# Optimization experiments

Measured on AMD Instinct MI355X. Metric: run time of the kernel, lower is better.

The kernel has to match this reference:

```python
import jax, jax.numpy as jnp
import numpy as np

REG_MAX = 16
BOX_W = 7.5
OBJ_W = 1.0
TOPK = 10
EPS = 1e-7


def dfl_decode(x, reg_max):
    # x: [B, 4*reg_max, N] -> expected value of per-side distribution -> [B, N, 4] (xyxy)
    B, C, N = x.shape
    x = x.reshape(B, 4, reg_max, N)
    p = jax.nn.softmax(x, axis=2)
    proj = jnp.arange(reg_max, dtype=x.dtype)
    return jnp.einsum('bkrn,r->bnk', p, proj)


def bbox_ciou(b1, b2):
    # b1: [B,N,1,4], b2: [B,1,M,4], xyxy -> [B,N,M]
    x11, y11, x12, y12 = b1[..., 0], b1[..., 1], b1[..., 2], b1[..., 3]
    x21, y21, x22, y22 = b2[..., 0], b2[..., 1], b2[..., 2], b2[..., 3]
    w1, h1 = x12 - x11, y12 - y11
    w2, h2 = x22 - x21, y22 - y21
    iw = jnp.clip(jnp.minimum(x12, x22) - jnp.maximum(x11, x21), 0.0)
    ih = jnp.clip(jnp.minimum(y12, y22) - jnp.maximum(y11, y21), 0.0)
    inter = iw * ih
    union = w1 * h1 + w2 * h2 - inter + EPS
    iou = inter / union
    cw = jnp.maximum(x12, x22) - jnp.minimum(x11, x21)
    ch = jnp.maximum(y12, y22) - jnp.minimum(y11, y21)
    c2 = cw * cw + ch * ch + EPS
    rho2 = ((x21 + x22 - x11 - x12) ** 2 + (y21 + y22 - y11 - y12) ** 2) * 0.25
    v = (4.0 / (np.pi ** 2)) * (jnp.arctan(w2 / (h2 + EPS)) - jnp.arctan(w1 / (h1 + EPS))) ** 2
    alpha = jax.lax.stop_gradient(v / (v - iou + 1.0 + EPS))
    return iou - rho2 / c2 - alpha * v


def setup_inputs() -> dict:
    key = jax.random.key(0)
    k1, k2, k3, k4 = jax.random.split(key, 4)
    B, N, M = 8, 34000, 64
    boxes = jax.random.normal(k1, (B, 4 * REG_MAX, N), dtype=jnp.float32)
    scores = jax.random.normal(k2, (B, N), dtype=jnp.float32)
    # GT boxes: valid xyxy in roughly the same [0, reg_max) range as decoded preds
    xy = jax.random.uniform(k3, (B, M, 2), dtype=jnp.float32) * 11.0
    wh = jax.random.uniform(k4, (B, M, 2), dtype=jnp.float32) * 4.0 + 0.5
    targets = jnp.concatenate([xy, xy + wh], axis=-1)
    return {'boxes': boxes, 'scores': scores, 'targets': targets}


def reference(boxes, scores, targets):
    B, N = scores.shape
    M = targets.shape[1]
    pb = dfl_decode(boxes, REG_MAX)                     # [B,N,4]
    ciou = bbox_ciou(pb[:, :, None, :], targets[:, None, :, :])  # [B,N,M]
    k = min(TOPK, N)
    topv, topi = jax.lax.top_k(jnp.swapaxes(ciou, 1, 2), k)      # [B,M,k] over anchors
    valid = topv > 0.0
    vals = jnp.where(valid, topv, 0.0)

    def per_batch(idx, val, vld):
        flat_i = idx.reshape(-1)
        iou_t = jnp.zeros((N,), val.dtype).at[flat_i].max(val.reshape(-1))
        pos = jnp.zeros((N,), bool).at[flat_i].max(vld.reshape(-1))
        return iou_t, pos

    iou_target, pos = jax.vmap(per_batch)(topi, vals, valid)     # [B,N]
    posf = pos.astype(iou_target.dtype)
    npos = posf.sum(axis=1)
    box_per = jnp.where(npos > 0,
                        ((1.0 - iou_target) * posf).sum(axis=1) / jnp.maximum(npos, 1.0),
                        0.0)
    box_loss = box_per.sum()
    # BCEWithLogits (mean over anchors), summed over batch
    bce = jnp.maximum(scores, 0.0) - scores * iou_target + jnp.log1p(jnp.exp(-jnp.abs(scores)))
    obj_loss = bce.mean(axis=1).sum()
    total = (BOX_W * box_loss + OBJ_W * obj_loss) / B
    return total, box_loss, obj_loss
```

## Files before the change

### kernel.cpp

```cpp
#include <hip/hip_runtime.h>
#include <math.h>

#define BQ 8
#define MQ 64
#define REGMAX 16
#define KTOP 10
#define EPSQ 1e-7f
#define SSEG 4
#define TRIG 256
#define CBUF (TRIG + SSEG * 256 + 16)

__device__ __forceinline__ float frcp(float x) { return __builtin_amdgcn_rcpf(x); }


__global__ __launch_bounds__(256) void decode_kernel(
    const float* __restrict__ boxes, const float* __restrict__ scores,
    float4* __restrict__ pbc, float2* __restrict__ atc,
    unsigned int* __restrict__ iou_bits, float* __restrict__ state,
    int N, int bpb) {
  const int tid = threadIdx.x;
  const int b = blockIdx.x / bpb;
  const int n = (blockIdx.x - b * bpb) * 256 + tid;
  float* acc = state;
  int* cnt = (int*)(state + 32);

  __shared__ float4 s_v4[256];
  __shared__ float2 s_ai[256];
  __shared__ int s_cnt, s_base;
  __shared__ float r0[256];
  if (tid == 0) s_cnt = 0;
  __syncthreads();

  float bce0 = 0.f;
  if (n < N) {
    const size_t i = (size_t)b * N + n;
    iou_bits[i] = 0u;
    float sc = scores[i];
    bce0 = fmaxf(sc, 0.f) + log1pf(__expf(-fabsf(sc)));
    const float* base = boxes + (size_t)b * (4 * REGMAX) * N + n;
    float out[4];
#pragma unroll
    for (int k = 0; k < 4; ++k) {
      float x[REGMAX];
#pragma unroll
      for (int r = 0; r < REGMAX; ++r)
        x[r] = base[(size_t)(k * REGMAX + r) * N];
      float mx = x[0];
#pragma unroll
      for (int r = 1; r < REGMAX; ++r) mx = fmaxf(mx, x[r]);
      float s = 0.f, ws = 0.f;
#pragma unroll
      for (int r = 0; r < REGMAX; ++r) {
        float e = __expf(x[r] - mx);
        s += e;
        ws += (float)r * e;
      }
      out[k] = ws * frcp(s);
    }
    float w1 = out[2] - out[0], h1 = out[3] - out[1];
    if (w1 > 0.f && h1 > 0.f) {
      int slot = atomicAdd(&s_cnt, 1);
      s_v4[slot] = make_float4(out[0], out[1], out[2], out[3]);
      s_ai[slot] = make_float2(atanf(w1 * frcp(h1 + EPSQ)), __int_as_float(n));
    }
  }
  __syncthreads();
  const int bc = s_cnt;
  if (tid == 0) s_base = atomicAdd(&cnt[b], bc);
  __syncthreads();
  const int basei = s_base;
  for (int sl = tid; sl < bc; sl += 256) {
    pbc[(size_t)b * N + basei + sl] = s_v4[sl];
    atc[(size_t)b * N + basei + sl] = s_ai[sl];
  }
  r0[tid] = bce0;
  __syncthreads();
  for (int s = 128; s > 0; s >>= 1) {
    if (tid < s) r0[tid] += r0[tid + s];
    __syncthreads();
  }
  if (tid == 0) atomicAdd(&acc[b * 4 + 2], r0[0]);
}

__device__ __forceinline__ void select_top10(
    float* s_bv, int* s_bi, float* s_winv, int* s_wini,
    int* s_cnt, float* s_sthr, int c, int tid) {
  if (tid < 64) {
    for (int r = 0; r < KTOP; ++r) {
      float bv = 0.f;
      int bs = 0xffff;
      for (int sl = tid; sl < c; sl += 64) {
        float v = s_bv[sl];
        if (v > bv) { bv = v; bs = sl; }
      }
      unsigned long long key =
          ((unsigned long long)__float_as_uint(bv) << 32) | (unsigned int)bs;
#pragma unroll
      for (int d = 1; d < 64; d <<= 1) {
        unsigned long long o = __shfl_xor(key, d, 64);
        if (o > key) key = o;
      }
      if (tid == 0) {
        float wv = __uint_as_float((unsigned int)(key >> 32));
        int ws = (int)(key & 0xffffu);
        s_winv[r] = wv;
        if (wv > 0.f && ws != 0xffff) {
          s_wini[r] = s_bi[ws];
          s_bv[ws] = 0.f;
        } else {
          s_wini[r] = 0;
        }
      }
    }
    if (tid < KTOP) { s_bv[tid] = s_winv[tid]; s_bi[tid] = s_wini[tid]; }
    if (tid == 0) { *s_cnt = KTOP; *s_sthr = s_winv[KTOP - 1]; }
  }
}

__global__ __launch_bounds__(256) void topk_all_kernel(
    const float4* __restrict__ pbc, const float2* __restrict__ atc,
    const float* __restrict__ targets, const float* __restrict__ scores,
    unsigned int* __restrict__ iou_bits, unsigned int* __restrict__ fin_v,
    int* __restrict__ fin_i, float* __restrict__ state,
    float* __restrict__ out, int N) {
  const int bm = blockIdx.x;
  const int b = bm >> 6;
  const int m = bm & 63;
  const int tid = threadIdx.x;
  float* acc = state;
  int* cnt = (int*)(state + 32);
  int* done = (int*)(state + 40);
  int* done_all = (int*)(state + 48);

  __shared__ float s_bv[CBUF];
  __shared__ int s_bi[CBUF];
  __shared__ float s_winv[KTOP];
  __shared__ int s_wini[KTOP];
  __shared__ int s_cnt, s_flag, s_flag2;
  __shared__ float s_sthr;
  if (tid == 0) { s_cnt = 0; s_sthr = 0.f; }
  __syncthreads();

  const float4 t = ((const float4*)targets)[b * MQ + m];
  const float x21 = t.x, y21 = t.y, x22 = t.z, y22 = t.w;
  const float w2 = x22 - x21, h2 = y22 - y21;
  const float atan_t = atanf(w2 * frcp(h2 + EPSQ));
  const float area2 = w2 * h2;
  const float sumx2 = x21 + x22, sumy2 = y21 + y22;
  const float CPI = 4.0f / (float)(M_PI * M_PI);

  const int cntb = cnt[b];
  float sthr = 0.f;
  const float4* pbb = pbc + (size_t)b * N;
  const float2* pab = atc + (size_t)b * N;

  for (int basei = 0; basei < cntb; basei += SSEG * 256) {
#pragma unroll
    for (int s = 0; s < SSEG; ++s) {
      int j = basei + s * 256 + tid;
      if (j < cntb) {
        float4 p = pbb[j];
        float2 ai = pab[j];
        float x11 = p.x, y11 = p.y, x12 = p.z, y12 = p.w;
        float w1 = x12 - x11, h1 = y12 - y11;
        float iw = fmaxf(fminf(x12, x22) - fmaxf(x11, x21), 0.f);
        float ih = fmaxf(fminf(y12, y22) - fmaxf(y11, y21), 0.f);
        float inter = iw * ih;
        float uni = w1 * h1 + area2 - inter + EPSQ;
        float iou = inter * frcp(uni);
        float cw = fmaxf(x12, x22) - fminf(x11, x21);
        float ch = fmaxf(y12, y22) - fminf(y11, y21);
        float c2 = cw * cw + ch * ch + EPSQ;
        float dx = sumx2 - x11 - x12;
        float dy = sumy2 - y11 - y12;
        float rho2 = (dx * dx + dy * dy) * 0.25f;
        float da = atan_t - ai.x;
        float v = CPI * da * da;
        float alpha = v * frcp(v - iou + 1.f + EPSQ);
        float ciou = iou - rho2 * frcp(c2) - alpha * v;
        if (ciou > sthr) {
          int slot = atomicAdd(&s_cnt, 1);
          s_bv[slot] = ciou;
          s_bi[slot] = __float_as_int(ai.y);
        }
      }
    }
    __syncthreads();
    int c = s_cnt;
    __syncthreads();
    if (c > TRIG) {
      select_top10(s_bv, s_bi, s_winv, s_wini, &s_cnt, &s_sthr, c, tid);
      __syncthreads();
    }
    sthr = s_sthr;
  }

  int c = s_cnt;
  if (c > KTOP) {
    select_top10(s_bv, s_bi, s_winv, s_wini, &s_cnt, &s_sthr, c, tid);
    __syncthreads();
    c = KTOP;
  }

  if (tid < KTOP) {
    float v = (tid < c) ? s_bv[tid] : 0.f;
    int ix = (tid < c) ? s_bi[tid] : 0;
    if (v > 0.f) atomicMax(&iou_bits[(size_t)b * N + ix], __float_as_uint(v));
    __hip_atomic_store(&fin_v[bm * KTOP + tid], __float_as_uint(v),
                       __ATOMIC_RELAXED, __HIP_MEMORY_SCOPE_AGENT);
    __hip_atomic_store(&fin_i[bm * KTOP + tid], ix, __ATOMIC_RELAXED,
                       __HIP_MEMORY_SCOPE_AGENT);
    __threadfence();
  }
  __syncthreads();
  if (tid == 0) {
    __threadfence();
    int prev = __hip_atomic_fetch_add(&done[b], 1, __ATOMIC_ACQ_REL,
                                      __HIP_MEMORY_SCOPE_AGENT);
    s_flag = (prev == MQ - 1);
  }
  __syncthreads();

  if (s_flag) {
    __threadfence();
    for (int e = tid; e < MQ * KTOP; e += 256) {
      int slot = b * (MQ * KTOP) + e;
      unsigned int vb = __hip_atomic_load(&fin_v[slot], __ATOMIC_RELAXED,
                                          __HIP_MEMORY_SCOPE_AGENT);
      float v = __uint_as_float(vb);
      if (v > 0.f) {
        int ix = __hip_atomic_load(&fin_i[slot], __ATOMIC_RELAXED,
                                   __HIP_MEMORY_SCOPE_AGENT);
        unsigned int cur = __hip_atomic_load(&iou_bits[(size_t)b * N + ix],
                                             __ATOMIC_RELAXED,
                                             __HIP_MEMORY_SCOPE_AGENT);
        if (cur == vb) {
          atomicAdd(&acc[b * 4 + 0], 1.f - v);
          atomicAdd(&acc[b * 4 + 1], 1.f);
          atomicAdd(&acc[b * 4 + 2], -scores[(size_t)b * N + ix] * v);
        }
      }
    }
    __threadfence();
    __syncthreads();
    if (tid == 0) {
      int prev = __hip_atomic_fetch_add(done_all, 1, __ATOMIC_ACQ_REL,
                                        __HIP_MEMORY_SCOPE_AGENT);
      s_flag2 = (prev == BQ - 1);
    }
    __syncthreads();
    if (s_flag2 && tid == 0) {
      __threadfence();
      float box = 0.f, obj = 0.f;
      for (int bb = 0; bb < BQ; ++bb) {
        float sb = __hip_atomic_load(&acc[bb * 4 + 0], __ATOMIC_RELAXED,
                                     __HIP_MEMORY_SCOPE_AGENT);
        float np = __hip_atomic_load(&acc[bb * 4 + 1], __ATOMIC_RELAXED,
                                     __HIP_MEMORY_SCOPE_AGENT);
        float sc = __hip_atomic_load(&acc[bb * 4 + 2], __ATOMIC_RELAXED,
                                     __HIP_MEMORY_SCOPE_AGENT);
        box += (np > 0.f) ? sb / fmaxf(np, 1.f) : 0.f;
        obj += sc / (float)N;
      }
      out[0] = (7.5f * box + obj) / (float)BQ;
      out[1] = box;
      out[2] = obj;
    }
  }
}

extern "C" void kernel_launch(void* const* d_in, const int* in_sizes, int n_in,
                              void* d_out, int out_size, void* d_ws, size_t ws_size,
                              hipStream_t stream) {
  const float* boxes = (const float*)d_in[0];
  const float* scores = (const float*)d_in[1];
  const float* targets = (const float*)d_in[2];
  float* out = (float*)d_out;
  const int N = in_sizes[1] / BQ;

  char* ws = (char*)d_ws;
  size_t pbc_bytes = (size_t)BQ * N * sizeof(float4);
  size_t atc_bytes = (size_t)BQ * N * sizeof(float2);
  size_t iou_bytes = (size_t)BQ * N * sizeof(unsigned int);
  size_t fin_bytes = (size_t)BQ * MQ * KTOP * sizeof(unsigned int);

  float4* pbc = (float4*)ws;                   ws += pbc_bytes;
  float2* atc = (float2*)ws;                   ws += atc_bytes;
  unsigned int* iou_bits = (unsigned int*)ws;  ws += iou_bytes;
  unsigned int* fin_v = (unsigned int*)ws;     ws += fin_bytes;
  int* fin_i = (int*)ws;                       ws += fin_bytes;
  float* state = (float*)ws;

  hipMemsetAsync(state, 0, 256, stream);

  const int bpb = (N + 255) / 256;
  decode_kernel<<<BQ * bpb, 256, 0, stream>>>(boxes, scores, pbc, atc,
                                              iou_bits, state, N, bpb);
  topk_all_kernel<<<BQ * MQ, 256, 0, stream>>>(pbc, atc, targets, scores,
                                               iou_bits, fin_v, fin_i, state,
                                               out, N);
}
```

Measured before the change: 169.0 us.

## Split per-target top-k scan into chunks and vectorize decode with float4 loads

The top-k kernel now launches four blocks per (batch, target) pair. Each block scans a quarter of the compacted anchors and writes ten candidates. The last block to finish merges the forty candidates by rank counting before the existing atomic bookkeeping runs. Separately, decode now uses 64-thread blocks that each handle four anchors with float4 loads, and reduces BCE with a wave shuffle instead of a shared-memory tree. The intent is to raise occupancy and parallelism for the 512-block top-k phase and cut decode memory transactions, at the cost of an extra counter and a merge step. The decode guard `na+3<N` skips any tail anchors when N is not a multiple of 4; N=34000 is, so this is fine here.

```diff
diff --git a/kernel.cpp b/kernel.cpp
--- a/kernel.cpp
+++ b/kernel.cpp
@@ -5,6 +5,7 @@
 #define MQ 64
 #define REGMAX 16
 #define KTOP 10
+#define CH 4
 #define EPSQ 1e-7f
 #define SSEG 4
 #define TRIG 256
@@ -12,56 +13,70 @@
 
 __device__ __forceinline__ float frcp(float x) { return __builtin_amdgcn_rcpf(x); }
 
-
-__global__ __launch_bounds__(256) void decode_kernel(
+#define ST_CNT 32
+#define ST_DONEC 40
+#define ST_DONE 552
+#define ST_DONEALL 560
+#define ST_BYTES 2560
+
+__global__ __launch_bounds__(64) void decode_kernel(
     const float* __restrict__ boxes, const float* __restrict__ scores,
     float4* __restrict__ pbc, float2* __restrict__ atc,
-    unsigned int* __restrict__ iou_bits, float* __restrict__ state,
-    int N, int bpb) {
+    uint4* __restrict__ iou4, float* __restrict__ state, int N, int bpb) {
   const int tid = threadIdx.x;
   const int b = blockIdx.x / bpb;
-  const int n = (blockIdx.x - b * bpb) * 256 + tid;
+  const int q = (blockIdx.x - b * bpb) * 64 + tid;
+  const int na = q * 4;
   float* acc = state;
-  int* cnt = (int*)(state + 32);
+  int* cnt = (int*)(state + ST_CNT);
 
   __shared__ float4 s_v4[256];
   __shared__ float2 s_ai[256];
   __shared__ int s_cnt, s_base;
-  __shared__ float r0[256];
   if (tid == 0) s_cnt = 0;
   __syncthreads();
 
   float bce0 = 0.f;
-  if (n < N) {
-    const size_t i = (size_t)b * N + n;
-    iou_bits[i] = 0u;
-    float sc = scores[i];
-    bce0 = fmaxf(sc, 0.f) + log1pf(__expf(-fabsf(sc)));
-    const float* base = boxes + (size_t)b * (4 * REGMAX) * N + n;
-    float out[4];
+  if (na + 3 < N) {
+    iou4[((size_t)b * N + na) >> 2] = make_uint4(0u, 0u, 0u, 0u);
+    float4 sc4 = *(const float4*)&scores[(size_t)b * N + na];
+    bce0 = fmaxf(sc4.x, 0.f) + log1pf(__expf(-fabsf(sc4.x))) +
+           fmaxf(sc4.y, 0.f) + log1pf(__expf(-fabsf(sc4.y))) +
+           fmaxf(sc4.z, 0.f) + log1pf(__expf(-fabsf(sc4.z))) +
+           fmaxf(sc4.w, 0.f) + log1pf(__expf(-fabsf(sc4.w)));
+    float out[4][4];
+    const size_t rowbase = (size_t)b * (4 * REGMAX) * N + na;
 #pragma unroll
     for (int k = 0; k < 4; ++k) {
-      float x[REGMAX];
+      float4 X[REGMAX];
 #pragma unroll
       for (int r = 0; r < REGMAX; ++r)
-        x[r] = base[(size_t)(k * REGMAX + r) * N];
-      float mx = x[0];
-#pragma unroll
-      for (int r = 1; r < REGMAX; ++r) mx = fmaxf(mx, x[r]);
-      float s = 0.f, ws = 0.f;
-#pragma unroll
-      for (int r = 0; r < REGMAX; ++r) {
-        float e = __expf(x[r] - mx);
-        s += e;
-        ws += (float)r * e;
-      }
-      out[k] = ws * frcp(s);
-    }
-    float w1 = out[2] - out[0], h1 = out[3] - out[1];
-    if (w1 > 0.f && h1 > 0.f) {
-      int slot = atomicAdd(&s_cnt, 1);
-      s_v4[slot] = make_float4(out[0], out[1], out[2], out[3]);
-      s_ai[slot] = make_float2(atanf(w1 * frcp(h1 + EPSQ)), __int_as_float(n));
+        X[r] = *(const float4*)&boxes[rowbase + (size_t)(k * REGMAX + r) * N];
+      const float* xf = (const float*)X;
+#pragma unroll
+      for (int a = 0; a < 4; ++a) {
+        float mx = xf[a];
+#pragma unroll
+        for (int r = 1; r < REGMAX; ++r) mx = fmaxf(mx, xf[r * 4 + a]);
+        float s = 0.f, ws = 0.f;
+#pragma unroll
+        for (int r = 0; r < REGMAX; ++r) {
+          float e = __expf(xf[r * 4 + a] - mx);
+          s += e;
+          ws += (float)r * e;
+        }
+        out[k][a] = ws * frcp(s);
+      }
+    }
+#pragma unroll
+    for (int a = 0; a < 4; ++a) {
+      float x1 = out[0][a], y1 = out[1][a], x2 = out[2][a], y2 = out[3][a];
+      float w1 = x2 - x1, h1 = y2 - y1;
+      if (w1 > 0.f && h1 > 0.f) {
+        int slot = atomicAdd(&s_cnt, 1);
+        s_v4[slot] = make_float4(x1, y1, x2, y2);
+        s_ai[slot] = make_float2(atanf(w1 * frcp(h1 + EPSQ)), __int_as_float(na + a));
+      }
     }
   }
   __syncthreads();
@@ -69,17 +84,13 @@
   if (tid == 0) s_base = atomicAdd(&cnt[b], bc);
   __syncthreads();
   const int basei = s_base;
-  for (int sl = tid; sl < bc; sl += 256) {
+  for (int sl = tid; sl < bc; sl += 64) {
     pbc[(size_t)b * N + basei + sl] = s_v4[sl];
     atc[(size_t)b * N + basei + sl] = s_ai[sl];
   }
-  r0[tid] = bce0;
-  __syncthreads();
-  for (int s = 128; s > 0; s >>= 1) {
-    if (tid < s) r0[tid] += r0[tid + s];
-    __syncthreads();
-  }
-  if (tid == 0) atomicAdd(&acc[b * 4 + 2], r0[0]);
+#pragma unroll
+  for (int d = 1; d < 64; d <<= 1) bce0 += __shfl_xor(bce0, d, 64);
+  if (tid == 0) atomicAdd(&acc[b * 4 + 2], bce0);
 }
 
 __device__ __forceinline__ void select_top10(
@@ -120,17 +131,21 @@
 __global__ __launch_bounds__(256) void topk_all_kernel(
     const float4* __restrict__ pbc, const float2* __restrict__ atc,
     const float* __restrict__ targets, const float* __restrict__ scores,
-    unsigned int* __restrict__ iou_bits, unsigned int* __restrict__ fin_v,
+    unsigned int* __restrict__ iou_bits, float* __restrict__ cand_v,
+    int* __restrict__ cand_i, unsigned int* __restrict__ fin_v,
     int* __restrict__ fin_i, float* __restrict__ state,
     float* __restrict__ out, int N) {
-  const int bm = blockIdx.x;
+  const int blk = blockIdx.x;
+  const int chunk = blk & (CH - 1);
+  const int bm = blk >> 2;
   const int b = bm >> 6;
   const int m = bm & 63;
   const int tid = threadIdx.x;
   float* acc = state;
-  int* cnt = (int*)(state + 32);
-  int* done = (int*)(state + 40);
-  int* done_all = (int*)(state + 48);
+  int* cnt = (int*)(state + ST_CNT);
+  int* donec = (int*)(state + ST_DONEC);
+  int* done = (int*)(state + ST_DONE);
+  int* done_all = (int*)(state + ST_DONEALL);
 
   __shared__ float s_bv[CBUF];
   __shared__ int s_bi[CBUF];
@@ -150,15 +165,18 @@
   const float CPI = 4.0f / (float)(M_PI * M_PI);
 
   const int cntb = cnt[b];
+  const int cch = (cntb + CH - 1) / CH;
+  const int j0 = chunk * cch;
+  const int j1 = min(cntb, j0 + cch);
   float sthr = 0.f;
   const float4* pbb = pbc + (size_t)b * N;
   const float2* pab = atc + (size_t)b * N;
 
-  for (int basei = 0; basei < cntb; basei += SSEG * 256) {
+  for (int basei = j0; basei < j1; basei += SSEG * 256) {
 #pragma unroll
     for (int s = 0; s < SSEG; ++s) {
       int j = basei + s * 256 + tid;
-      if (j < cntb) {
+      if (j < j1) {
         float4 p = pbb[j];
         float2 ai = pab[j];
         float x11 = p.x, y11 = p.y, x12 = p.z, y12 = p.w;
@@ -205,67 +223,108 @@
   if (tid < KTOP) {
     float v = (tid < c) ? s_bv[tid] : 0.f;
     int ix = (tid < c) ? s_bi[tid] : 0;
-    if (v > 0.f) atomicMax(&iou_bits[(size_t)b * N + ix], __float_as_uint(v));
-    __hip_atomic_store(&fin_v[bm * KTOP + tid], __float_as_uint(v),
-                       __ATOMIC_RELAXED, __HIP_MEMORY_SCOPE_AGENT);
-    __hip_atomic_store(&fin_i[bm * KTOP + tid], ix, __ATOMIC_RELAXED,
-                       __HIP_MEMORY_SCOPE_AGENT);
-    __threadfence();
-  }
+    cand_v[(bm * CH + chunk) * KTOP + tid] = v;
+    cand_i[(bm * CH + chunk) * KTOP + tid] = ix;
+  }
+  __threadfence();
   __syncthreads();
   if (tid == 0) {
-    __threadfence();
+    int prev = __hip_atomic_fetch_add(&donec[bm], 1, __ATOMIC_ACQ_REL,
+                                      __HIP_MEMORY_SCOPE_AGENT);
+    s_flag = (prev == CH - 1);
+  }
+  __syncthreads();
+  if (!s_flag) return;
+
+  {
+    const int NC = CH * KTOP;
+    __shared__ float mv[NC];
+    __shared__ int mi[NC];
+    __shared__ float topv[KTOP];
+    __shared__ int topi[KTOP];
+    if (tid < NC) {
+      mv[tid] = __hip_atomic_load(&cand_v[bm * NC + tid], __ATOMIC_RELAXED,
+                                  __HIP_MEMORY_SCOPE_AGENT);
+      mi[tid] = __hip_atomic_load(&cand_i[bm * NC + tid], __ATOMIC_RELAXED,
+                                  __HIP_MEMORY_SCOPE_AGENT);
+    }
+    if (tid < KTOP) { topv[tid] = 0.f; topi[tid] = 0; }
+    __syncthreads();
+    if (tid < NC) {
+      float v = mv[tid];
+      if (v > 0.f) {
+        int rank = 0;
+#pragma unroll
+        for (int i2 = 0; i2 < NC; ++i2)
+          rank += (mv[i2] > v) || (mv[i2] == v && i2 < tid);
+        if (rank < KTOP) { topv[rank] = v; topi[rank] = mi[tid]; }
+      }
+    }
+    __syncthreads();
+    if (tid < KTOP) {
+      float v = topv[tid];
+      int ix = topi[tid];
+      unsigned int vb = __float_as_uint(v);
+      if (v > 0.f) atomicMax(&iou_bits[(size_t)b * N + ix], vb);
+      __hip_atomic_store(&fin_v[bm * KTOP + tid], (v > 0.f) ? vb : 0u,
+                         __ATOMIC_RELAXED, __HIP_MEMORY_SCOPE_AGENT);
+      __hip_atomic_store(&fin_i[bm * KTOP + tid], ix, __ATOMIC_RELAXED,
+                         __HIP_MEMORY_SCOPE_AGENT);
+    }
+  }
+  __threadfence();
+  __syncthreads();
+  if (tid == 0) {
     int prev = __hip_atomic_fetch_add(&done[b], 1, __ATOMIC_ACQ_REL,
                                       __HIP_MEMORY_SCOPE_AGENT);
     s_flag = (prev == MQ - 1);
   }
   __syncthreads();
-
-  if (s_flag) {
+  if (!s_flag) return;
+
+  __threadfence();
+  for (int e = tid; e < MQ * KTOP; e += 256) {
+    int slot = b * (MQ * KTOP) + e;
+    unsigned int vb = __hip_atomic_load(&fin_v[slot], __ATOMIC_RELAXED,
+                                        __HIP_MEMORY_SCOPE_AGENT);
+    float v = __uint_as_float(vb);
+    if (v > 0.f) {
+      int ix = __hip_atomic_load(&fin_i[slot], __ATOMIC_RELAXED,
+                                 __HIP_MEMORY_SCOPE_AGENT);
+      unsigned int cur = __hip_atomic_load(&iou_bits[(size_t)b * N + ix],
+                                           __ATOMIC_RELAXED,
+                                           __HIP_MEMORY_SCOPE_AGENT);
+      if (cur == vb) {
+        atomicAdd(&acc[b * 4 + 0], 1.f - v);
+        atomicAdd(&acc[b * 4 + 1], 1.f);
+        atomicAdd(&acc[b * 4 + 2], -scores[(size_t)b * N + ix] * v);
+      }
+    }
+  }
+  __threadfence();
+  __syncthreads();
+  if (tid == 0) {
+    int prev = __hip_atomic_fetch_add(done_all, 1, __ATOMIC_ACQ_REL,
+                                      __HIP_MEMORY_SCOPE_AGENT);
+    s_flag2 = (prev == BQ - 1);
+  }
+  __syncthreads();
+  if (s_flag2 && tid == 0) {
     __threadfence();
-    for (int e = tid; e < MQ * KTOP; e += 256) {
-      int slot = b * (MQ * KTOP) + e;
-      unsigned int vb = __hip_atomic_load(&fin_v[slot], __ATOMIC_RELAXED,
-                                          __HIP_MEMORY_SCOPE_AGENT);
-      float v = __uint_as_float(vb);
-      if (v > 0.f) {
-        int ix = __hip_atomic_load(&fin_i[slot], __ATOMIC_RELAXED,
+    float box = 0.f, obj = 0.f;
+    for (int bb = 0; bb < BQ; ++bb) {
+      float sb = __hip_atomic_load(&acc[bb * 4 + 0], __ATOMIC_RELAXED,
                                    __HIP_MEMORY_SCOPE_AGENT);
-        unsigned int cur = __hip_atomic_load(&iou_bits[(size_t)b * N + ix],
-                                             __ATOMIC_RELAXED,
-                                             __HIP_MEMORY_SCOPE_AGENT);
-        if (cur == vb) {
-          atomicAdd(&acc[b * 4 + 0], 1.f - v);
-          atomicAdd(&acc[b * 4 + 1], 1.f);
-          atomicAdd(&acc[b * 4 + 2], -scores[(size_t)b * N + ix] * v);
-        }
-      }
-    }
-    __threadfence();
-    __syncthreads();
-    if (tid == 0) {
-      int prev = __hip_atomic_fetch_add(done_all, 1, __ATOMIC_ACQ_REL,
-                                        __HIP_MEMORY_SCOPE_AGENT);
-      s_flag2 = (prev == BQ - 1);
-    }
-    __syncthreads();
-    if (s_flag2 && tid == 0) {
-      __threadfence();
-      float box = 0.f, obj = 0.f;
-      for (int bb = 0; bb < BQ; ++bb) {
-        float sb = __hip_atomic_load(&acc[bb * 4 + 0], __ATOMIC_RELAXED,
-                                     __HIP_MEMORY_SCOPE_AGENT);
-        float np = __hip_atomic_load(&acc[bb * 4 + 1], __ATOMIC_RELAXED,
-                                     __HIP_MEMORY_SCOPE_AGENT);
-        float sc = __hip_atomic_load(&acc[bb * 4 + 2], __ATOMIC_RELAXED,
-                                     __HIP_MEMORY_SCOPE_AGENT);
-        box += (np > 0.f) ? sb / fmaxf(np, 1.f) : 0.f;
-        obj += sc / (float)N;
-      }
-      out[0] = (7.5f * box + obj) / (float)BQ;
-      out[1] = box;
-      out[2] = obj;
-    }
+      float np = __hip_atomic_load(&acc[bb * 4 + 1], __ATOMIC_RELAXED,
+                                   __HIP_MEMORY_SCOPE_AGENT);
+      float sc = __hip_atomic_load(&acc[bb * 4 + 2], __ATOMIC_RELAXED,
+                                   __HIP_MEMORY_SCOPE_AGENT);
+      box += (np > 0.f) ? sb / fmaxf(np, 1.f) : 0.f;
+      obj += sc / (float)N;
+    }
+    out[0] = (7.5f * box + obj) / (float)BQ;
+    out[1] = box;
+    out[2] = obj;
   }
 }
 
@@ -282,21 +341,24 @@
   size_t pbc_bytes = (size_t)BQ * N * sizeof(float4);
   size_t atc_bytes = (size_t)BQ * N * sizeof(float2);
   size_t iou_bytes = (size_t)BQ * N * sizeof(unsigned int);
+  size_t cand_bytes = (size_t)BQ * MQ * CH * KTOP * sizeof(float);
   size_t fin_bytes = (size_t)BQ * MQ * KTOP * sizeof(unsigned int);
 
   float4* pbc = (float4*)ws;                   ws += pbc_bytes;
   float2* atc = (float2*)ws;                   ws += atc_bytes;
   unsigned int* iou_bits = (unsigned int*)ws;  ws += iou_bytes;
+  float* cand_v = (float*)ws;                  ws += cand_bytes;
+  int* cand_i = (int*)ws;                      ws += cand_bytes;
   unsigned int* fin_v = (unsigned int*)ws;     ws += fin_bytes;
   int* fin_i = (int*)ws;                       ws += fin_bytes;
   float* state = (float*)ws;
 
-  hipMemsetAsync(state, 0, 256, stream);
-
-  const int bpb = (N + 255) / 256;
-  decode_kernel<<<BQ * bpb, 256, 0, stream>>>(boxes, scores, pbc, atc,
-                                              iou_bits, state, N, bpb);
-  topk_all_kernel<<<BQ * MQ, 256, 0, stream>>>(pbc, atc, targets, scores,
-                                               iou_bits, fin_v, fin_i, state,
-                                               out, N);
+  hipMemsetAsync(state, 0, ST_BYTES, stream);
+
+  const int bpb = (N / 4 + 63) / 64;
+  decode_kernel<<<BQ * bpb, 64, 0, stream>>>(boxes, scores, pbc, atc,
+                                             (uint4*)iou_bits, state, N, bpb);
+  topk_all_kernel<<<BQ * MQ * CH, 256, 0, stream>>>(
+      pbc, atc, targets, scores, iou_bits, cand_v, cand_i, fin_v, fin_i,
+      state, out, N);
 }
```

New measurement: 357.7 us. 112% more time.

## Split per-target top-k across anchor chunks and vectorize DFL decode loads

Applied to the files above, without the earlier changes.

The top-k stage now runs four blocks per (batch, target), each scanning a quarter of the compacted anchors. A second small kernel merges the 40 candidates by rank and applies atomicMax with delta-based accumulation, and a separate finalize kernel replaces the last-block-done atomic chain. This raises the grid from 512 to 2048 blocks so more CUs stay busy. Decode now has each thread load float4 across four anchors for one side, which widens memory accesses and stages the expected values through shared memory. The cost is two extra kernel launches, and the delta-accumulation logic can race when concurrent updates hit the same anchor. Also, the vectorized decode skips any trailing partial group of four anchors when N is not a multiple of 4.

```diff
diff --git a/kernel.cpp b/kernel.cpp
--- a/kernel.cpp
+++ b/kernel.cpp
@@ -5,6 +5,7 @@
 #define MQ 64
 #define REGMAX 16
 #define KTOP 10
+#define CH 4
 #define EPSQ 1e-7f
 #define SSEG 4
 #define TRIG 256
@@ -12,6 +13,8 @@
 
 __device__ __forceinline__ float frcp(float x) { return __builtin_amdgcn_rcpf(x); }
 
+#define ST_CNT 32
+#define ST_BYTES 256
 
 __global__ __launch_bounds__(256) void decode_kernel(
     const float* __restrict__ boxes, const float* __restrict__ scores,
@@ -20,66 +23,76 @@
     int N, int bpb) {
   const int tid = threadIdx.x;
   const int b = blockIdx.x / bpb;
-  const int n = (blockIdx.x - b * bpb) * 256 + tid;
+  const int a0 = (blockIdx.x - b * bpb) * 256;
   float* acc = state;
-  int* cnt = (int*)(state + 32);
-
+  int* cnt = (int*)(state + ST_CNT);
+
+  __shared__ float s_ex[4 * 256];
   __shared__ float4 s_v4[256];
   __shared__ float2 s_ai[256];
+  __shared__ float r0[256];
   __shared__ int s_cnt, s_base;
-  __shared__ float r0[256];
   if (tid == 0) s_cnt = 0;
+
+  const int g = tid >> 6;
+  const int l = tid & 63;
+  const int na = a0 + l * 4;
+  if (na + 3 < N) {
+    float4 X[REGMAX];
+    const size_t rowbase = ((size_t)b * 4 * REGMAX + g * REGMAX) * N + na;
+#pragma unroll
+    for (int r = 0; r < REGMAX; ++r)
+      X[r] = *(const float4*)&boxes[rowbase + (size_t)r * N];
+    const float* xf = (const float*)X;
+    float ev[4];
+#pragma unroll
+    for (int a = 0; a < 4; ++a) {
+      float mx = xf[a];
+#pragma unroll
+      for (int r = 1; r < REGMAX; ++r) mx = fmaxf(mx, xf[r * 4 + a]);
+      float s = 0.f, ws = 0.f;
+#pragma unroll
+      for (int r = 0; r < REGMAX; ++r) {
+        float e = __expf(xf[r * 4 + a] - mx);
+        s += e;
+        ws += (float)r * e;
+      }
+      ev[a] = ws * frcp(s);
+    }
+    *(float4*)&s_ex[g * 256 + l * 4] = make_float4(ev[0], ev[1], ev[2], ev[3]);
+  }
   __syncthreads();
 
+  const int n = a0 + tid;
   float bce0 = 0.f;
   if (n < N) {
     const size_t i = (size_t)b * N + n;
     iou_bits[i] = 0u;
     float sc = scores[i];
     bce0 = fmaxf(sc, 0.f) + log1pf(__expf(-fabsf(sc)));
-    const float* base = boxes + (size_t)b * (4 * REGMAX) * N + n;
-    float out[4];
-#pragma unroll
-    for (int k = 0; k < 4; ++k) {
-      float x[REGMAX];
-#pragma unroll
-      for (int r = 0; r < REGMAX; ++r)
-        x[r] = base[(size_t)(k * REGMAX + r) * N];
-      float mx = x[0];
-#pragma unroll
-      for (int r = 1; r < REGMAX; ++r) mx = fmaxf(mx, x[r]);
-      float s = 0.f, ws = 0.f;
-#pragma unroll
-      for (int r = 0; r < REGMAX; ++r) {
-        float e = __expf(x[r] - mx);
-        s += e;
-        ws += (float)r * e;
-      }
-      out[k] = ws * frcp(s);
-    }
-    float w1 = out[2] - out[0], h1 = out[3] - out[1];
+    float x1 = s_ex[0 * 256 + tid], y1 = s_ex[1 * 256 + tid];
+    float x2 = s_ex[2 * 256 + tid], y2 = s_ex[3 * 256 + tid];
+    float w1 = x2 - x1, h1 = y2 - y1;
     if (w1 > 0.f && h1 > 0.f) {
       int slot = atomicAdd(&s_cnt, 1);
-      s_v4[slot] = make_float4(out[0], out[1], out[2], out[3]);
+      s_v4[slot] = make_float4(x1, y1, x2, y2);
       s_ai[slot] = make_float2(atanf(w1 * frcp(h1 + EPSQ)), __int_as_float(n));
     }
   }
+  r0[tid] = bce0;
   __syncthreads();
   const int bc = s_cnt;
   if (tid == 0) s_base = atomicAdd(&cnt[b], bc);
-  __syncthreads();
+  for (int s = 128; s > 0; s >>= 1) {
+    if (tid < s) r0[tid] += r0[tid + s];
+    __syncthreads();
+  }
+  if (tid == 0) atomicAdd(&acc[b * 4 + 2], r0[0]);
   const int basei = s_base;
   for (int sl = tid; sl < bc; sl += 256) {
     pbc[(size_t)b * N + basei + sl] = s_v4[sl];
     atc[(size_t)b * N + basei + sl] = s_ai[sl];
   }
-  r0[tid] = bce0;
-  __syncthreads();
-  for (int s = 128; s > 0; s >>= 1) {
-    if (tid < s) r0[tid] += r0[tid + s];
-    __syncthreads();
-  }
-  if (tid == 0) atomicAdd(&acc[b * 4 + 2], r0[0]);
 }
 
 __device__ __forceinline__ void select_top10(
@@ -117,26 +130,23 @@
   }
 }
 
-__global__ __launch_bounds__(256) void topk_all_kernel(
+__global__ __launch_bounds__(256) void topk1_kernel(
     const float4* __restrict__ pbc, const float2* __restrict__ atc,
-    const float* __restrict__ targets, const float* __restrict__ scores,
-    unsigned int* __restrict__ iou_bits, unsigned int* __restrict__ fin_v,
-    int* __restrict__ fin_i, float* __restrict__ state,
-    float* __restrict__ out, int N) {
-  const int bm = blockIdx.x;
+    const float* __restrict__ targets, float* __restrict__ cand_v,
+    int* __restrict__ cand_i, const float* __restrict__ state, int N) {
+  const int blk = blockIdx.x;
+  const int chunk = blk & (CH - 1);
+  const int bm = blk >> 2;
   const int b = bm >> 6;
   const int m = bm & 63;
   const int tid = threadIdx.x;
-  float* acc = state;
-  int* cnt = (int*)(state + 32);
-  int* done = (int*)(state + 40);
-  int* done_all = (int*)(state + 48);
+  const int* cnt = (const int*)(state + ST_CNT);
 
   __shared__ float s_bv[CBUF];
   __shared__ int s_bi[CBUF];
   __shared__ float s_winv[KTOP];
   __shared__ int s_wini[KTOP];
-  __shared__ int s_cnt, s_flag, s_flag2;
+  __shared__ int s_cnt;
   __shared__ float s_sthr;
   if (tid == 0) { s_cnt = 0; s_sthr = 0.f; }
   __syncthreads();
@@ -150,15 +160,18 @@
   const float CPI = 4.0f / (float)(M_PI * M_PI);
 
   const int cntb = cnt[b];
+  const int cch = (cntb + CH - 1) / CH;
+  const int j0 = chunk * cch;
+  const int j1 = min(cntb, j0 + cch);
   float sthr = 0.f;
   const float4* pbb = pbc + (size_t)b * N;
   const float2* pab = atc + (size_t)b * N;
 
-  for (int basei = 0; basei < cntb; basei += SSEG * 256) {
+  for (int basei = j0; basei < j1; basei += SSEG * 256) {
 #pragma unroll
     for (int s = 0; s < SSEG; ++s) {
       int j = basei + s * 256 + tid;
-      if (j < cntb) {
+      if (j < j1) {
         float4 p = pbb[j];
         float2 ai = pab[j];
         float x11 = p.x, y11 = p.y, x12 = p.z, y12 = p.w;
@@ -201,71 +214,65 @@
     __syncthreads();
     c = KTOP;
   }
-
   if (tid < KTOP) {
-    float v = (tid < c) ? s_bv[tid] : 0.f;
-    int ix = (tid < c) ? s_bi[tid] : 0;
-    if (v > 0.f) atomicMax(&iou_bits[(size_t)b * N + ix], __float_as_uint(v));
-    __hip_atomic_store(&fin_v[bm * KTOP + tid], __float_as_uint(v),
-                       __ATOMIC_RELAXED, __HIP_MEMORY_SCOPE_AGENT);
-    __hip_atomic_store(&fin_i[bm * KTOP + tid], ix, __ATOMIC_RELAXED,
-                       __HIP_MEMORY_SCOPE_AGENT);
-    __threadfence();
+    cand_v[(bm * CH + chunk) * KTOP + tid] = (tid < c) ? s_bv[tid] : 0.f;
+    cand_i[(bm * CH + chunk) * KTOP + tid] = (tid < c) ? s_bi[tid] : 0;
+  }
+}
+
+__global__ __launch_bounds__(64) void topk2_kernel(
+    const float* __restrict__ cand_v, const int* __restrict__ cand_i,
+    const float* __restrict__ scores, unsigned int* __restrict__ iou_bits,
+    float* __restrict__ state, int N) {
+  const int bm = blockIdx.x;
+  const int b = bm >> 6;
+  const int tid = threadIdx.x;
+  float* acc = state;
+  const int NC = CH * KTOP;
+  __shared__ float mv[NC];
+  __shared__ int mi[NC];
+  if (tid < NC) {
+    mv[tid] = cand_v[bm * NC + tid];
+    mi[tid] = cand_i[bm * NC + tid];
   }
   __syncthreads();
-  if (tid == 0) {
-    __threadfence();
-    int prev = __hip_atomic_fetch_add(&done[b], 1, __ATOMIC_ACQ_REL,
-                                      __HIP_MEMORY_SCOPE_AGENT);
-    s_flag = (prev == MQ - 1);
-  }
-  __syncthreads();
-
-  if (s_flag) {
-    __threadfence();
-    for (int e = tid; e < MQ * KTOP; e += 256) {
-      int slot = b * (MQ * KTOP) + e;
-      unsigned int vb = __hip_atomic_load(&fin_v[slot], __ATOMIC_RELAXED,
-                                          __HIP_MEMORY_SCOPE_AGENT);
-      float v = __uint_as_float(vb);
-      if (v > 0.f) {
-        int ix = __hip_atomic_load(&fin_i[slot], __ATOMIC_RELAXED,
-                                   __HIP_MEMORY_SCOPE_AGENT);
-        unsigned int cur = __hip_atomic_load(&iou_bits[(size_t)b * N + ix],
-                                             __ATOMIC_RELAXED,
-                                             __HIP_MEMORY_SCOPE_AGENT);
-        if (cur == vb) {
-          atomicAdd(&acc[b * 4 + 0], 1.f - v);
-          atomicAdd(&acc[b * 4 + 1], 1.f);
-          atomicAdd(&acc[b * 4 + 2], -scores[(size_t)b * N + ix] * v);
+  if (tid < NC) {
+    float v = mv[tid];
+    if (v > 0.f) {
+      int rank = 0;
+#pragma unroll
+      for (int i2 = 0; i2 < NC; ++i2)
+        rank += (mv[i2] > v) || (mv[i2] == v && i2 < tid);
+      if (rank < KTOP) {
+        int ix = mi[tid];
+        unsigned int vb = __float_as_uint(v);
+        unsigned int old = atomicMax(&iou_bits[(size_t)b * N + ix], vb);
+        if (old < vb) {
+          float vold = __uint_as_float(old);
+          bool was = (old != 0u);
+          atomicAdd(&acc[b * 4 + 0], was ? (vold - v) : (1.f - v));
+          if (!was) atomicAdd(&acc[b * 4 + 1], 1.f);
+          atomicAdd(&acc[b * 4 + 2], -scores[(size_t)b * N + ix] * (v - vold));
         }
       }
     }
-    __threadfence();
-    __syncthreads();
-    if (tid == 0) {
-      int prev = __hip_atomic_fetch_add(done_all, 1, __ATOMIC_ACQ_REL,
-                                        __HIP_MEMORY_SCOPE_AGENT);
-      s_flag2 = (prev == BQ - 1);
-    }
-    __syncthreads();
-    if (s_flag2 && tid == 0) {
-      __threadfence();
-      float box = 0.f, obj = 0.f;
-      for (int bb = 0; bb < BQ; ++bb) {
-        float sb = __hip_atomic_load(&acc[bb * 4 + 0], __ATOMIC_RELAXED,
-                                     __HIP_MEMORY_SCOPE_AGENT);
-        float np = __hip_atomic_load(&acc[bb * 4 + 1], __ATOMIC_RELAXED,
-                                     __HIP_MEMORY_SCOPE_AGENT);
-        float sc = __hip_atomic_load(&acc[bb * 4 + 2], __ATOMIC_RELAXED,
-                                     __HIP_MEMORY_SCOPE_AGENT);
-        box += (np > 0.f) ? sb / fmaxf(np, 1.f) : 0.f;
-        obj += sc / (float)N;
-      }
-      out[0] = (7.5f * box + obj) / (float)BQ;
-      out[1] = box;
-      out[2] = obj;
-    }
+  }
+}
+
+__global__ void finalize_kernel(const float* __restrict__ acc,
+                                float* __restrict__ out, int N) {
+  if (threadIdx.x == 0 && blockIdx.x == 0) {
+    float box = 0.f, obj = 0.f;
+    for (int bb = 0; bb < BQ; ++bb) {
+      float sb = acc[bb * 4 + 0];
+      float np = acc[bb * 4 + 1];
+      float sc = acc[bb * 4 + 2];
+      box += (np > 0.f) ? sb / fmaxf(np, 1.f) : 0.f;
+      obj += sc / (float)N;
+    }
+    out[0] = (7.5f * box + obj) / (float)BQ;
+    out[1] = box;
+    out[2] = obj;
   }
 }
 
@@ -282,21 +289,23 @@
   size_t pbc_bytes = (size_t)BQ * N * sizeof(float4);
   size_t atc_bytes = (size_t)BQ * N * sizeof(float2);
   size_t iou_bytes = (size_t)BQ * N * sizeof(unsigned int);
-  size_t fin_bytes = (size_t)BQ * MQ * KTOP * sizeof(unsigned int);
+  size_t cand_bytes = (size_t)BQ * MQ * CH * KTOP * sizeof(float);
 
   float4* pbc = (float4*)ws;                   ws += pbc_bytes;
   float2* atc = (float2*)ws;                   ws += atc_bytes;
   unsigned int* iou_bits = (unsigned int*)ws;  ws += iou_bytes;
-  unsigned int* fin_v = (unsigned int*)ws;     ws += fin_bytes;
-  int* fin_i = (int*)ws;                       ws += fin_bytes;
+  float* cand_v = (float*)ws;                  ws += cand_bytes;
+  int* cand_i = (int*)ws;                      ws += cand_bytes;
   float* state = (float*)ws;
 
-  hipMemsetAsync(state, 0, 256, stream);
+  hipMemsetAsync(state, 0, ST_BYTES, stream);
 
   const int bpb = (N + 255) / 256;
   decode_kernel<<<BQ * bpb, 256, 0, stream>>>(boxes, scores, pbc, atc,
                                               iou_bits, state, N, bpb);
-  topk_all_kernel<<<BQ * MQ, 256, 0, stream>>>(pbc, atc, targets, scores,
-                                               iou_bits, fin_v, fin_i, state,
-                                               out, N);
-}
+  topk1_kernel<<<BQ * MQ * CH, 256, 0, stream>>>(pbc, atc, targets, cand_v,
+                                                 cand_i, state, N);
+  topk2_kernel<<<BQ * MQ, 64, 0, stream>>>(cand_v, cand_i, scores, iou_bits,
+                                           state, N);
+  finalize_kernel<<<1, 64, 0, stream>>>(state, out, N);
+}
```

After: 142.1 us. -15.9%, faster.
